# Kernel tuning notes

Measured on AMD Instinct MI355X. Metric: run time of the kernel, lower is better.

Reference implementation:

```python
import jax, jax.numpy as jnp
import numpy as np

EPS = 1e-6
P = 0.8
NUM_CLASSES = 1604
BATCH = 16384


def _make_seesaw_matrix(key, num_classes, p):
    # Synthetic long-tailed class counts standing in for the CSV bincount.
    counts = jax.random.randint(key, (num_classes,), 1, 10000).astype(jnp.float32)
    cond = counts[:, None] > counts[None, :]
    ratio = (counts[None, :] / counts[:, None]) ** p
    return jnp.where(cond, ratio, jnp.ones_like(ratio))  # [C, C]


def setup_inputs() -> dict:
    key = jax.random.key(0)
    k_log, k_tgt, k_cnt = jax.random.split(key, 3)
    logits = jax.random.normal(k_log, (BATCH, NUM_CLASSES), dtype=jnp.float32)
    targets = jax.random.randint(k_tgt, (BATCH,), 0, NUM_CLASSES)
    s = _make_seesaw_matrix(k_cnt, NUM_CLASSES, P)
    return {"logits": logits, "s": s, "targets": targets}


def reference(logits, s, targets):
    # logits: [B, C], s: [C, C], targets: [B] int
    C = s.shape[0]
    onehot = jax.nn.one_hot(targets, C, dtype=logits.dtype)  # [B, C]
    logits = logits - jnp.max(logits, axis=-1, keepdims=True)
    numerator = jnp.exp(logits)  # [B, C]
    # denom[b, i] = sum_j (1 - t[b, j]) * s[i, j] * exp(logits[b, j]) + exp(logits[b, i])
    # Expressed as a GEMM instead of the original [B, C, C] broadcast.
    denominator = jnp.einsum('bj,ij->bi', (1.0 - onehot) * numerator, s) + numerator
    sigma = numerator / (denominator + EPS)
    loss = -(onehot * jnp.log(sigma + EPS)).sum(axis=-1)  # [B]
    return loss.mean()
```

## Files before the change

kernel.cpp:

```cpp
#include <hip/hip_runtime.h>
#include <math.h>

#define EPS 1e-6f
#define C 1604
#define B 16384
#define C4 401
#define BLOCK 256
#define ROWS_PER_BLOCK 4
#define TAIL_LANES (C4 - 6 * 64)

__global__ __launch_bounds__(BLOCK) void seesaw_row_kernel(
    const float* __restrict__ logits,
    const float* __restrict__ s,
    const int*   __restrict__ targets,
    float*       __restrict__ row_loss)
{
    const int wave = threadIdx.x >> 6;
    const int lane = threadIdx.x & 63;
    const int b = blockIdx.x * ROWS_PER_BLOCK + wave;
    const int t = targets[b];

    const float4* lrow = (const float4*)(logits + (size_t)b * C);
    const float4* srow = (const float4*)(s + (size_t)t * C);

    float4 lv[7], sv[7];
    #pragma unroll
    for (int k = 0; k < 6; ++k) lv[k] = lrow[lane + 64 * k];
    #pragma unroll
    for (int k = 0; k < 6; ++k) sv[k] = srow[lane + 64 * k];
    const bool tail = lane < TAIL_LANES;
    lv[6] = tail ? lrow[lane + 384]
                 : make_float4(-INFINITY, -INFINITY, -INFINITY, -INFINITY);
    sv[6] = tail ? srow[lane + 384] : make_float4(0.f, 0.f, 0.f, 0.f);

    float m = -INFINITY;
    #pragma unroll
    for (int k = 0; k < 7; ++k)
        m = fmaxf(m, fmaxf(fmaxf(lv[k].x, lv[k].y), fmaxf(lv[k].z, lv[k].w)));
    #pragma unroll
    for (int off = 32; off > 0; off >>= 1)
        m = fmaxf(m, __shfl_xor(m, off, 64));

    float p = 0.f;
    float lt_local = 0.f;
    #pragma unroll
    for (int k = 0; k < 7; ++k) {
        const int j = (lane + 64 * k) << 2;
        const bool e0 = (j     == t);
        const bool e1 = (j + 1 == t);
        const bool e2 = (j + 2 == t);
        const bool e3 = (j + 3 == t);
        p += __expf(lv[k].x - m) * (e0 ? 1.f : sv[k].x);
        p += __expf(lv[k].y - m) * (e1 ? 1.f : sv[k].y);
        p += __expf(lv[k].z - m) * (e2 ? 1.f : sv[k].z);
        p += __expf(lv[k].w - m) * (e3 ? 1.f : sv[k].w);
        if (e0) lt_local = lv[k].x;
        if (e1) lt_local = lv[k].y;
        if (e2) lt_local = lv[k].z;
        if (e3) lt_local = lv[k].w;
    }
    #pragma unroll
    for (int off = 32; off > 0; off >>= 1)
        p += __shfl_xor(p, off, 64);

    const float lt = __shfl(lt_local, (t >> 2) & 63, 64);

    if (lane == 0) {
        const float numt  = __expf(lt - m);
        const float sigma = numt / (p + EPS);
        row_loss[b] = -logf(sigma + EPS);
    }
}

__global__ __launch_bounds__(1024) void seesaw_reduce_kernel(
    const float* __restrict__ in, float* __restrict__ out)
{
    const int tid = threadIdx.x;
    const float4* in4 = (const float4*)in;
    float acc = 0.f;
    #pragma unroll
    for (int i = tid; i < B / 4; i += 1024) {
        float4 v = in4[i];
        acc += (v.x + v.y) + (v.z + v.w);
    }
    #pragma unroll
    for (int off = 32; off > 0; off >>= 1)
        acc += __shfl_xor(acc, off, 64);
    __shared__ float sw[16];
    if ((tid & 63) == 0) sw[tid >> 6] = acc;
    __syncthreads();
    if (tid == 0) {
        float s0 = 0.f;
        #pragma unroll
        for (int w = 0; w < 16; ++w) s0 += sw[w];
        out[0] = s0 * (1.0f / B);
    }
}

extern "C" void kernel_launch(void* const* d_in, const int* in_sizes, int n_in,
                              void* d_out, int out_size, void* d_ws, size_t ws_size,
                              hipStream_t stream) {
    const float* logits  = (const float*)d_in[0];
    const float* s       = (const float*)d_in[1];
    const int*   targets = (const int*)d_in[2];
    float* out      = (float*)d_out;
    float* row_loss = (float*)d_ws;

    seesaw_row_kernel<<<B / ROWS_PER_BLOCK, BLOCK, 0, stream>>>(logits, s, targets, row_loss);
    seesaw_reduce_kernel<<<1, 1024, 0, stream>>>(row_loss, out);
}
```

Baseline: 163.9 us.

## Fuse row loss and mean reduction via bucketed atomics and last-block finish

Merges the per-row loss kernel and the separate reduction kernel into one launch. Each block sums its four row losses, atomically adds the sum into one of 64 buckets, and the last block to finish, found with an atomic counter, reduces the buckets and writes the mean. Logits loads also become nontemporal to avoid polluting cache. This removes the second kernel launch and the row_loss round trip, but adds a memset per call, atomic contention on the buckets, and a nondeterministic floating-point summation order.

```diff
diff --git a/kernel.cpp b/kernel.cpp
--- a/kernel.cpp
+++ b/kernel.cpp
@@ -5,33 +5,43 @@
 #define C 1604
 #define B 16384
 #define C4 401
+#define ROWS_PER_BLOCK 4
 #define BLOCK 256
-#define ROWS_PER_BLOCK 4
+#define GRID (B / ROWS_PER_BLOCK)
+#define NBUCKETS 64
 #define TAIL_LANES (C4 - 6 * 64)
 
-__global__ __launch_bounds__(BLOCK) void seesaw_row_kernel(
+typedef __attribute__((ext_vector_type(4))) float f32x4;
+
+__global__ __launch_bounds__(BLOCK) void seesaw_fused_kernel(
     const float* __restrict__ logits,
     const float* __restrict__ s,
     const int*   __restrict__ targets,
-    float*       __restrict__ row_loss)
+    float*       __restrict__ out,
+    float*       __restrict__ buckets,
+    unsigned int* __restrict__ counter)
 {
     const int wave = threadIdx.x >> 6;
     const int lane = threadIdx.x & 63;
     const int b = blockIdx.x * ROWS_PER_BLOCK + wave;
     const int t = targets[b];
 
-    const float4* lrow = (const float4*)(logits + (size_t)b * C);
-    const float4* srow = (const float4*)(s + (size_t)t * C);
+    const f32x4* lrow = (const f32x4*)(logits + (size_t)b * C);
+    const f32x4* srow = (const f32x4*)(s + (size_t)t * C);
 
-    float4 lv[7], sv[7];
+    f32x4 lv[7], sv[7];
     #pragma unroll
-    for (int k = 0; k < 6; ++k) lv[k] = lrow[lane + 64 * k];
+    for (int k = 0; k < 6; ++k) lv[k] = __builtin_nontemporal_load(&lrow[lane + 64 * k]);
     #pragma unroll
     for (int k = 0; k < 6; ++k) sv[k] = srow[lane + 64 * k];
     const bool tail = lane < TAIL_LANES;
-    lv[6] = tail ? lrow[lane + 384]
-                 : make_float4(-INFINITY, -INFINITY, -INFINITY, -INFINITY);
-    sv[6] = tail ? srow[lane + 384] : make_float4(0.f, 0.f, 0.f, 0.f);
+    if (tail) {
+        lv[6] = __builtin_nontemporal_load(&lrow[lane + 384]);
+        sv[6] = srow[lane + 384];
+    } else {
+        lv[6] = (f32x4){-INFINITY, -INFINITY, -INFINITY, -INFINITY};
+        sv[6] = (f32x4){0.f, 0.f, 0.f, 0.f};
+    }
 
     float m = -INFINITY;
     #pragma unroll
@@ -65,35 +75,31 @@
 
     const float lt = __shfl(lt_local, (t >> 2) & 63, 64);
 
+    __shared__ float wsum[ROWS_PER_BLOCK];
+    __shared__ int   s_last;
     if (lane == 0) {
         const float numt  = __expf(lt - m);
         const float sigma = numt / (p + EPS);
-        row_loss[b] = -logf(sigma + EPS);
+        wsum[wave] = -logf(sigma + EPS);
     }
-}
+    __syncthreads();
+    if (threadIdx.x == 0) {
+        const float bsum = (wsum[0] + wsum[1]) + (wsum[2] + wsum[3]);
+        atomicAdd(&buckets[blockIdx.x & (NBUCKETS - 1)], bsum);
+        __threadfence();
+        const unsigned old = atomicAdd(counter, 1u);
+        s_last = (old == GRID - 1);
+    }
+    __syncthreads();
 
-__global__ __launch_bounds__(1024) void seesaw_reduce_kernel(
-    const float* __restrict__ in, float* __restrict__ out)
-{
-    const int tid = threadIdx.x;
-    const float4* in4 = (const float4*)in;
-    float acc = 0.f;
-    #pragma unroll
-    for (int i = tid; i < B / 4; i += 1024) {
-        float4 v = in4[i];
-        acc += (v.x + v.y) + (v.z + v.w);
-    }
-    #pragma unroll
-    for (int off = 32; off > 0; off >>= 1)
-        acc += __shfl_xor(acc, off, 64);
-    __shared__ float sw[16];
-    if ((tid & 63) == 0) sw[tid >> 6] = acc;
-    __syncthreads();
-    if (tid == 0) {
-        float s0 = 0.f;
+    if (s_last && wave == 0) {
+        float v = __hip_atomic_load(&buckets[lane], __ATOMIC_RELAXED,
+                                    __HIP_MEMORY_SCOPE_AGENT);
         #pragma unroll
-        for (int w = 0; w < 16; ++w) s0 += sw[w];
-        out[0] = s0 * (1.0f / B);
+        for (int off = 32; off > 0; off >>= 1)
+            v += __shfl_xor(v, off, 64);
+        if (lane == 0)
+            out[0] = v * (1.0f / B);
     }
 }
 
@@ -103,9 +109,12 @@
     const float* logits  = (const float*)d_in[0];
     const float* s       = (const float*)d_in[1];
     const int*   targets = (const int*)d_in[2];
-    float* out      = (float*)d_out;
-    float* row_loss = (float*)d_ws;
+    float* out = (float*)d_out;
 
-    seesaw_row_kernel<<<B / ROWS_PER_BLOCK, BLOCK, 0, stream>>>(logits, s, targets, row_loss);
-    seesaw_reduce_kernel<<<1, 1024, 0, stream>>>(row_loss, out);
+    float* buckets        = (float*)d_ws;
+    unsigned int* counter = (unsigned int*)((char*)d_ws + 256);
+
+    hipMemsetAsync(d_ws, 0, 512, stream);
+    seesaw_fused_kernel<<<GRID, BLOCK, 0, stream>>>(logits, s, targets, out,
+                                                    buckets, counter);
 }
```

Result: slower. 346.3 us (+111.3%).
